# Performance work log

Hardware: AMD Instinct MI355X
Metric: run time of the kernel (lower is better)

## Reference

```python
import jax, jax.numpy as jnp
import numpy as np

B, N, DIM = 16, 784, 512
H, KD, VD = 8, 64, 256  # num_heads, key_dim, val_dim (attn_ratio=4)
RES = 28
EPS = 1e-5
SCALE = KD ** -0.5


def _make_bias_idxs():
    # pos: [2, N] grid coordinates; rel_pos[0]*RES + rel_pos[1]
    yy, xx = np.meshgrid(np.arange(RES), np.arange(RES), indexing='ij')
    pos = np.stack([yy.reshape(-1), xx.reshape(-1)])  # [2, N]
    rel = np.abs(pos[:, :, None] - pos[:, None, :])   # [2, N, N]
    return jnp.asarray(rel[0] * RES + rel[1], dtype=jnp.int32)


def _bn(x, gamma, beta, mean, var):
    return (x - mean) * (gamma * jax.lax.rsqrt(var + EPS)) + beta


def setup_inputs() -> dict:
    key = jax.random.key(0)
    ks = jax.random.split(key, 12)
    qkv_out = (2 * KD + VD) * H  # 3072
    return {
        'x': jax.random.normal(ks[0], (B, N, DIM), jnp.float32),
        'qkv_w': jax.random.normal(ks[1], (qkv_out, DIM), jnp.float32) * (DIM ** -0.5),
        'qkv_gamma': jax.random.uniform(ks[2], (qkv_out,), jnp.float32, 0.5, 1.5),
        'qkv_beta': jax.random.normal(ks[3], (qkv_out,), jnp.float32) * 0.1,
        'qkv_mean': jax.random.normal(ks[4], (qkv_out,), jnp.float32) * 0.1,
        'qkv_var': jax.random.uniform(ks[5], (qkv_out,), jnp.float32, 0.5, 1.5),
        'attention_biases': jax.random.normal(ks[6], (H, RES * RES), jnp.float32) * 0.02,
        'proj_w': jax.random.normal(ks[7], (DIM, VD * H), jnp.float32) * ((VD * H) ** -0.5),
        'proj_gamma': jax.random.uniform(ks[8], (DIM,), jnp.float32, 0.5, 1.5),
        'proj_beta': jax.random.normal(ks[9], (DIM,), jnp.float32) * 0.1,
        'proj_mean': jax.random.normal(ks[10], (DIM,), jnp.float32) * 0.1,
        'proj_var': jax.random.uniform(ks[11], (DIM,), jnp.float32, 0.5, 1.5),
        'bias_idxs': _make_bias_idxs(),
    }


def reference(x, qkv_w, qkv_gamma, qkv_beta, qkv_mean, qkv_var,
              attention_biases, proj_w, proj_gamma, proj_beta,
              proj_mean, proj_var, bias_idxs):
    # QKV: Linear (no bias) + BatchNorm1d (eval/fused form)
    qkv = _bn(jnp.einsum('bnc,oc->bno', x, qkv_w),
              qkv_gamma, qkv_beta, qkv_mean, qkv_var)        # [B, N, 3072]
    qkv = qkv.reshape(B, N, H, 2 * KD + VD)
    q = qkv[..., :KD].transpose(0, 2, 1, 3)                  # [B, H, N, KD]
    k = qkv[..., KD:2 * KD].transpose(0, 2, 1, 3)            # [B, H, N, KD]
    v = qkv[..., 2 * KD:].transpose(0, 2, 1, 3)              # [B, H, N, VD]

    bias = attention_biases[:, bias_idxs]                    # [H, N, N]
    attn = jnp.einsum('bhnd,bhmd->bhnm', q, k) * SCALE + bias
    attn = jax.nn.softmax(attn, axis=-1)
    out = jnp.einsum('bhnm,bhmd->bhnd', attn, v)             # [B, H, N, VD]
    out = out.transpose(0, 2, 1, 3).reshape(B, N, H * VD)    # [B, N, 2048]

    # proj: SiLU -> Linear (no bias) -> BN (eval/fused form)
    out = jax.nn.silu(out)
    out = _bn(jnp.einsum('bnv,cv->bnc', out, proj_w),
              proj_gamma, proj_beta, proj_mean, proj_var)    # [B, N, DIM]
    return out
```

## Files before the change

kernel.cpp:

```cpp
#include <hip/hip_runtime.h>

#define Bsz 16
#define Nseq 784
#define DIM 512
#define NH 8
#define KD 64
#define VD 256
#define QKV_OUT 3072
#define HV 2048
#define NN 614656

typedef __attribute__((ext_vector_type(8))) short short8;
typedef __attribute__((ext_vector_type(4))) float floatx4;

#define OSTR 136

#if __has_builtin(__builtin_amdgcn_exp2f)
#define EXP2(x) __builtin_amdgcn_exp2f(x)
#else
#define EXP2(x) exp2f(x)
#endif

__device__ __forceinline__ unsigned short f2bf(float f) {
  union { float f; unsigned u; } v; v.f = f;
  unsigned r = v.u + 0x7fffu + ((v.u >> 16) & 1u);
  return (unsigned short)(r >> 16);
}
__device__ __forceinline__ float bf2f(unsigned short u) {
  union { unsigned u; float f; } v; v.u = ((unsigned)u) << 16;
  return v.f;
}

__device__ __forceinline__ void glds16(const unsigned short* g, unsigned short* l) {
  __builtin_amdgcn_global_load_lds(
      (const __attribute__((address_space(1))) void*)g,
      (__attribute__((address_space(3))) void*)l, 16, 0, 0);
}

#define N4X 1605632
#define N4Q 393216
#define N4P 262144
__global__ void cvt_all_kernel(const float* __restrict__ x,
                               const float* __restrict__ qw,
                               const float* __restrict__ pw,
                               unsigned short* __restrict__ xb,
                               unsigned short* __restrict__ wq,
                               unsigned short* __restrict__ wp) {
  int i = blockIdx.x * 256 + threadIdx.x;
  const float4* s; ushort4* d; int off;
  if (i < N4X)              { s = (const float4*)x;  d = (ushort4*)xb; off = i; }
  else if (i < N4X + N4Q)   { s = (const float4*)qw; d = (ushort4*)wq; off = i - N4X; }
  else if (i < N4X + N4Q + N4P) { s = (const float4*)pw; d = (ushort4*)wp; off = i - N4X - N4Q; }
  else return;
  float4 v = s[off];
  ushort4 o;
  o.x = f2bf(v.x); o.y = f2bf(v.y); o.z = f2bf(v.z); o.w = f2bf(v.w);
  d[off] = o;
}

__global__ void bias_pre_kernel(const float* __restrict__ biases,
                                const int* __restrict__ bias_idxs,
                                unsigned short* __restrict__ bias_tab) {
  int t = blockIdx.x * 256 + threadIdx.x;
  if (t >= NN) return;
  int idx = bias_idxs[t];
  for (int h = 0; h < NH; ++h)
    bias_tab[(size_t)h * NN + t] = f2bf(biases[h * Nseq + idx]);
}

__global__ __launch_bounds__(256, 2) void qkv_gemm_kernel(
    const unsigned short* __restrict__ A,
    const unsigned short* __restrict__ Bw,
    const float* __restrict__ gamma, const float* __restrict__ beta,
    const float* __restrict__ mean,  const float* __restrict__ var,
    unsigned short* __restrict__ qo,
    unsigned short* __restrict__ ko,
    unsigned short* __restrict__ vto)
{
  const int K = DIM;
  __shared__ unsigned short smem[128 * OSTR];
  int tid = threadIdx.x;
  int wave = tid >> 6, lane = tid & 63;
  int quad = lane >> 4, l16 = lane & 15;
  int wm = wave >> 1, wn = wave & 1;
  int m0 = blockIdx.y * 128, n0 = blockIdx.x * 128;

  int srow = wave * 32 + (lane >> 2);
  int sch = (lane & 3) * 8;
  const unsigned short* Ab = A + (size_t)(m0 + srow) * K + sch;
  const unsigned short* Bb = Bw + (size_t)(n0 + srow) * K + sch;
  unsigned short* AsW = &smem[wave * 1024];
  unsigned short* BsW = &smem[4096 + wave * 1024];

  floatx4 acc[4][4];
  for (int i = 0; i < 4; ++i)
    for (int j = 0; j < 4; ++j) acc[i][j] = (floatx4)0.0f;

  glds16(Ab, AsW);
  glds16(Ab + 16 * K, AsW + 512);
  glds16(Bb, BsW);
  glds16(Bb + 16 * K, BsW + 512);

  for (int k = 0; k < 16; ++k) {
    int cur = k & 1, nb = cur ^ 1;
    __builtin_amdgcn_s_waitcnt(0xC07F);
    __builtin_amdgcn_s_barrier();
    int k0n = ((k + 1) & 15) * 32;
    glds16(Ab + k0n, AsW + nb * 8192);
    glds16(Ab + k0n + 16 * K, AsW + nb * 8192 + 512);
    glds16(Bb + k0n, BsW + nb * 8192);
    glds16(Bb + k0n + 16 * K, BsW + nb * 8192 + 512);
    __builtin_amdgcn_s_waitcnt(0x0F74);
    __builtin_amdgcn_s_barrier();

    const unsigned short* As = &smem[cur * 8192];
    const unsigned short* Bs = &smem[4096 + cur * 8192];
    short8 af[4], bfr[4];
    for (int mt = 0; mt < 4; ++mt)
      af[mt] = *(const short8*)&As[(wm * 64 + mt * 16 + l16) * 32 + quad * 8];
    for (int nt = 0; nt < 4; ++nt)
      bfr[nt] = *(const short8*)&Bs[(wn * 64 + nt * 16 + l16) * 32 + quad * 8];
    for (int mt = 0; mt < 4; ++mt)
      for (int nt = 0; nt < 4; ++nt)
        acc[mt][nt] = __builtin_amdgcn_mfma_f32_16x16x32_bf16(af[mt], bfr[nt], acc[mt][nt], 0, 0, 0);
  }

  int tt = n0 % 384;
  int h = n0 / 384;
  __builtin_amdgcn_s_waitcnt(0x0070);
  __syncthreads();

  if (tt == 0) {
    for (int nt = 0; nt < 4; ++nt) {
      int o = n0 + wn * 64 + nt * 16 + l16;
      float sc = gamma[o] * rsqrtf(var[o] + 1e-5f);
      float bb = beta[o] - mean[o] * sc;
      if (wn == 0) { sc *= 0.125f; bb *= 0.125f; }
      int jl = wn * 64 + nt * 16 + l16;
      for (int mt = 0; mt < 4; ++mt)
        for (int r = 0; r < 4; ++r) {
          int ml = wm * 64 + mt * 16 + quad * 4 + r;
          smem[ml * OSTR + jl] = f2bf(acc[mt][nt][r] * sc + bb);
        }
    }
    __syncthreads();
    for (int i = 0; i < 8; ++i) {
      int c = i * 256 + tid;
      int ml = c >> 4, jc = c & 15;
      int m = m0 + ml;
      int b = m / 784, n = m - b * 784;
      uint4 v = *(uint4*)&smem[ml * OSTR + jc * 8];
      int j = jc * 8;
      if (j < 64) *(uint4*)&qo[(((size_t)b * NH + h) * Nseq + n) * KD + j] = v;
      else        *(uint4*)&ko[(((size_t)b * NH + h) * Nseq + n) * KD + (j - 64)] = v;
    }
  } else {
    for (int nt = 0; nt < 4; ++nt) {
      int o = n0 + wn * 64 + nt * 16 + l16;
      float sc = gamma[o] * rsqrtf(var[o] + 1e-5f);
      float bb = beta[o] - mean[o] * sc;
      int cl = wn * 64 + nt * 16 + l16;
      for (int mt = 0; mt < 4; ++mt)
        for (int r = 0; r < 4; ++r) {
          int ml = wm * 64 + mt * 16 + quad * 4 + r;
          smem[cl * OSTR + ml] = f2bf(acc[mt][nt][r] * sc + bb);
        }
    }
    __syncthreads();
    int cbase = tt - 128;
    for (int i = 0; i < 8; ++i) {
      int c = i * 256 + tid;
      int cl = c >> 4, mc = c & 15;
      int m = m0 + mc * 8;
      int b = m / 784, n = m - b * 784;
      uint4 v = *(uint4*)&smem[cl * OSTR + mc * 8];
      *(uint4*)&vto[(((size_t)b * NH + h) * VD + cbase + cl) * Nseq + n] = v;
    }
  }
}

__global__ __launch_bounds__(512, 2) void attn_kernel(
    const unsigned short* __restrict__ qb,
    const unsigned short* __restrict__ kb,
    const unsigned short* __restrict__ vtb,
    const unsigned short* __restrict__ bias_tab,
    unsigned short* __restrict__ U)
{
  __shared__ unsigned short vt_lds[2 * 256 * 64];
  __shared__ unsigned short k_lds[2 * 64 * 64];
  __shared__ unsigned short bs_lds[2 * 128 * 64];
  __shared__ unsigned short ps_lds[8 * 16 * 64];
  int tid = threadIdx.x;
  int wave = tid >> 6, lane = tid & 63;
  int quad = lane >> 4, l16 = lane & 15;

  int L = blockIdx.x;
  int xcd = L & 7;
  int s = L >> 3;
  int qp = s % 7;
  int bg = s / 7;
  int bh = bg * 8 + xcd;
  int b = bg, h = xcd;
  int row_base = qp * 128 + wave * 16;

  const unsigned short* brow = bias_tab + (size_t)h * NN;

  int lc = lane >> 3;
  int lch = (lane & 7) ^ lc;
  int sw = l16 & 7;

  const unsigned short* vsrc[4];
#pragma unroll
  for (int t = 0; t < 4; ++t)
    vsrc[t] = vtb + ((size_t)bh * VD + t * 64 + wave * 8 + lc) * Nseq + lch * 8;
  const unsigned short* ksrc =
      kb + (size_t)bh * (Nseq * KD) + (wave * 8 + lc) * KD + lch * 8;
  const unsigned short* bsrc[2];
#pragma unroll
  for (int t = 0; t < 2; ++t) {
    int ig = qp * 128 + t * 64 + wave * 8 + lc;
    if (ig > Nseq - 1) ig = Nseq - 1;
    bsrc[t] = brow + (size_t)ig * Nseq + lch * 8;
  }

  short8 qf[2];
  {
    int qrow = row_base + l16;
    const unsigned short* qp_ = qb + ((size_t)bh * Nseq + qrow) * KD;
    qf[0] = *(const short8*)(qp_ + quad * 8);
    qf[1] = *(const short8*)(qp_ + 32 + quad * 8);
  }

#pragma unroll
  for (int t = 0; t < 4; ++t)
    glds16(vsrc[t], &vt_lds[(t * 64 + wave * 8) * 64]);
  glds16(ksrc, &k_lds[wave * 512]);
#pragma unroll
  for (int t = 0; t < 2; ++t)
    glds16(bsrc[t], &bs_lds[(t * 64 + wave * 8) * 64]);

  float lsum = 0.0f;
  floatx4 oacc[16];
#pragma unroll
  for (int ct = 0; ct < 16; ++ct) oacc[ct] = (floatx4)0.0f;

  unsigned short* psW = &ps_lds[wave * 1024];

  for (int kt = 0; kt < 13; ++kt) {
    int cur = kt & 1;
    int nb = cur ^ 1;
    __builtin_amdgcn_s_waitcnt(0xC07F);
    __builtin_amdgcn_s_barrier();

    int ktn = kt + 1; if (ktn >= 13) ktn = 0;
#pragma unroll
    for (int t = 0; t < 4; ++t)
      glds16(vsrc[t] + ktn * 64, &vt_lds[nb * 16384 + (t * 64 + wave * 8) * 64]);
    glds16(ksrc + (size_t)ktn * 4096, &k_lds[nb * 4096 + wave * 512]);
#pragma unroll
    for (int t = 0; t < 2; ++t)
      glds16(bsrc[t] + ktn * 64, &bs_lds[nb * 8192 + (t * 64 + wave * 8) * 64]);

    __builtin_amdgcn_s_waitcnt(0x0F77);
    __builtin_amdgcn_s_barrier();

    const unsigned short* kbuf = &k_lds[cur * 4096];
    const unsigned short* vbuf = &vt_lds[cur * 16384];
    const unsigned short* bbuf = &bs_lds[cur * 8192];

    floatx4 st[4];
#pragma unroll
    for (int jt = 0; jt < 4; ++jt) {
      int row = jt * 16 + l16;
      short8 kf0 = *(const short8*)&kbuf[row * 64 + (quad ^ sw) * 8];
      short8 kf1 = *(const short8*)&kbuf[row * 64 + ((quad + 4) ^ sw) * 8];
      st[jt] = (floatx4)0.0f;
      st[jt] = __builtin_amdgcn_mfma_f32_16x16x32_bf16(kf0, qf[0], st[jt], 0, 0, 0);
      st[jt] = __builtin_amdgcn_mfma_f32_16x16x32_bf16(kf1, qf[1], st[jt], 0, 0, 0);
    }

    bool tail = (kt == 12);
#pragma unroll
    for (int jt = 0; jt < 4; ++jt) {
      int ch = ((jt << 1) + (quad >> 1)) ^ sw;
      int half = (quad & 1) * 4;
      ushort4 bv = *(const ushort4*)&bbuf[(wave * 16 + l16) * 64 + ch * 8 + half];
      float p0 = EXP2((st[jt][0] + bf2f(bv.x)) * 1.44269504f);
      float p1 = EXP2((st[jt][1] + bf2f(bv.y)) * 1.44269504f);
      float p2 = EXP2((st[jt][2] + bf2f(bv.z)) * 1.44269504f);
      float p3 = EXP2((st[jt][3] + bf2f(bv.w)) * 1.44269504f);
      if (tail && jt > 0) { p0 = 0.0f; p1 = 0.0f; p2 = 0.0f; p3 = 0.0f; }
      lsum += (p0 + p1) + (p2 + p3);
      unsigned lo = (unsigned)f2bf(p0) | ((unsigned)f2bf(p1) << 16);
      unsigned hi = (unsigned)f2bf(p2) | ((unsigned)f2bf(p3) << 16);
      *(uint2*)&psW[l16 * 64 + ch * 8 + half] = make_uint2(lo, hi);
    }

#pragma unroll
    for (int ks = 0; ks < 2; ++ks) {
      short8 pf = *(const short8*)&psW[l16 * 64 + ((ks * 4 + quad) ^ sw) * 8];
#pragma unroll
      for (int ct = 0; ct < 16; ++ct) {
        int c = ct * 16 + l16;
        short8 vf = *(const short8*)&vbuf[c * 64 + ((ks * 4 + quad) ^ sw) * 8];
        oacc[ct] = __builtin_amdgcn_mfma_f32_16x16x32_bf16(pf, vf, oacc[ct], 0, 0, 0);
      }
    }
  }

  __builtin_amdgcn_s_waitcnt(0x0070);

  float tot = lsum;
  tot += __shfl_xor(tot, 16);
  tot += __shfl_xor(tot, 32);
  float inv[4];
#pragma unroll
  for (int r = 0; r < 4; ++r) {
    float lr = __shfl(tot, (lane & 48) | (quad * 4 + r));
    inv[r] = 1.0f / lr;
  }
#pragma unroll
  for (int r = 0; r < 4; ++r) {
    int ig = row_base + quad * 4 + r;
    if (ig >= Nseq) continue;
    size_t base = ((size_t)b * Nseq + ig) * HV + h * VD;
#pragma unroll
    for (int ct = 0; ct < 16; ++ct) {
      float u = oacc[ct][r] * inv[r];
      float sg = 1.0f / (1.0f + EXP2(-u * 1.44269504f));
      U[base + ct * 16 + l16] = f2bf(u * sg);
    }
  }
}

__global__ __launch_bounds__(256, 2) void proj_gemm_kernel(
    const unsigned short* __restrict__ Ubuf,
    const unsigned short* __restrict__ Wp,
    const float* __restrict__ gamma, const float* __restrict__ beta,
    const float* __restrict__ mean,  const float* __restrict__ var,
    float* __restrict__ out)
{
  const int K = HV;
  __shared__ unsigned short smem[16384];
  int tid = threadIdx.x;
  int wave = tid >> 6, lane = tid & 63;
  int quad = lane >> 4, l16 = lane & 15;
  int wm = wave >> 1, wn = wave & 1;
  int o0 = blockIdx.y * 128, mB = blockIdx.x * 128;

  int srow = wave * 32 + (lane >> 2);
  int sch = (lane & 3) * 8;
  const unsigned short* Ab = Wp + (size_t)(o0 + srow) * K + sch;
  const unsigned short* Bb = Ubuf + (size_t)(mB + srow) * K + sch;
  unsigned short* AsW = &smem[wave * 1024];
  unsigned short* BsW = &smem[4096 + wave * 1024];

  floatx4 acc[4][4];
  for (int i = 0; i < 4; ++i)
    for (int j = 0; j < 4; ++j) acc[i][j] = (floatx4)0.0f;

  glds16(Ab, AsW);
  glds16(Ab + 16 * K, AsW + 512);
  glds16(Bb, BsW);
  glds16(Bb + 16 * K, BsW + 512);

  for (int k = 0; k < 64; ++k) {
    int cur = k & 1, nb = cur ^ 1;
    __builtin_amdgcn_s_waitcnt(0xC07F);
    __builtin_amdgcn_s_barrier();
    int k0n = ((k + 1) & 63) * 32;
    glds16(Ab + k0n, AsW + nb * 8192);
    glds16(Ab + k0n + 16 * K, AsW + nb * 8192 + 512);
    glds16(Bb + k0n, BsW + nb * 8192);
    glds16(Bb + k0n + 16 * K, BsW + nb * 8192 + 512);
    __builtin_amdgcn_s_waitcnt(0x0F74);
    __builtin_amdgcn_s_barrier();

    const unsigned short* As = &smem[cur * 8192];
    const unsigned short* Bs = &smem[4096 + cur * 8192];
    short8 af[4], bfr[4];
    for (int mt = 0; mt < 4; ++mt)
      af[mt] = *(const short8*)&As[(wm * 64 + mt * 16 + l16) * 32 + quad * 8];
    for (int nt = 0; nt < 4; ++nt)
      bfr[nt] = *(const short8*)&Bs[(wn * 64 + nt * 16 + l16) * 32 + quad * 8];
    for (int mt = 0; mt < 4; ++mt)
      for (int nt = 0; nt < 4; ++nt)
        acc[mt][nt] = __builtin_amdgcn_mfma_f32_16x16x32_bf16(af[mt], bfr[nt], acc[mt][nt], 0, 0, 0);
  }
  __builtin_amdgcn_s_waitcnt(0x0070);

  for (int mt = 0; mt < 4; ++mt) {
    int ob = o0 + wm * 64 + mt * 16 + quad * 4;
    float4 g = *(const float4*)&gamma[ob];
    float4 vr = *(const float4*)&var[ob];
    float4 mn = *(const float4*)&mean[ob];
    float4 bt = *(const float4*)&beta[ob];
    float sc0 = g.x * rsqrtf(vr.x + 1e-5f), bb0 = bt.x - mn.x * sc0;
    float sc1 = g.y * rsqrtf(vr.y + 1e-5f), bb1 = bt.y - mn.y * sc1;
    float sc2 = g.z * rsqrtf(vr.z + 1e-5f), bb2 = bt.z - mn.z * sc2;
    float sc3 = g.w * rsqrtf(vr.w + 1e-5f), bb3 = bt.w - mn.w * sc3;
    for (int nt = 0; nt < 4; ++nt) {
      int m = mB + wn * 64 + nt * 16 + l16;
      float4 v;
      v.x = acc[mt][nt][0] * sc0 + bb0;
      v.y = acc[mt][nt][1] * sc1 + bb1;
      v.z = acc[mt][nt][2] * sc2 + bb2;
      v.w = acc[mt][nt][3] * sc3 + bb3;
      *(float4*)&out[(size_t)m * DIM + ob] = v;
    }
  }
}

extern "C" void kernel_launch(void* const* d_in, const int* in_sizes, int n_in,
                              void* d_out, int out_size, void* d_ws, size_t ws_size,
                              hipStream_t stream) {
  const float* x          = (const float*)d_in[0];
  const float* qkv_w      = (const float*)d_in[1];
  const float* qkv_gamma  = (const float*)d_in[2];
  const float* qkv_beta   = (const float*)d_in[3];
  const float* qkv_mean   = (const float*)d_in[4];
  const float* qkv_var    = (const float*)d_in[5];
  const float* att_biases = (const float*)d_in[6];
  const float* proj_w     = (const float*)d_in[7];
  const float* proj_gamma = (const float*)d_in[8];
  const float* proj_beta  = (const float*)d_in[9];
  const float* proj_mean  = (const float*)d_in[10];
  const float* proj_var   = (const float*)d_in[11];
  const int*   bias_idxs  = (const int*)d_in[12];
  float* out = (float*)d_out;

  char* ws = (char*)d_ws;
  unsigned short* xb  = (unsigned short*)(ws);
  unsigned short* bias_tab = (unsigned short*)(ws);
  unsigned short* wq  = (unsigned short*)(ws + 12845056);
  unsigned short* wp  = (unsigned short*)(ws + 15990784);
  unsigned short* qo  = (unsigned short*)(ws + 18087936);
  unsigned short* ko  = (unsigned short*)(ws + 30932992);
  unsigned short* vto = (unsigned short*)(ws + 43778048);
  unsigned short* Ub  = (unsigned short*)(ws + 95158272);

  {
    int n4 = N4X + N4Q + N4P;
    cvt_all_kernel<<<(n4 + 255) / 256, 256, 0, stream>>>(x, qkv_w, proj_w, xb, wq, wp);
  }

  qkv_gemm_kernel<<<dim3(QKV_OUT / 128, (Bsz * Nseq) / 128), 256, 0, stream>>>(
      xb, wq, qkv_gamma, qkv_beta, qkv_mean, qkv_var, qo, ko, vto);

  bias_pre_kernel<<<(NN + 255) / 256, 256, 0, stream>>>(att_biases, bias_idxs, bias_tab);

  attn_kernel<<<7 * Bsz * NH, 512, 0, stream>>>(qo, ko, vto, bias_tab, Ub);

  proj_gemm_kernel<<<dim3((Bsz * Nseq) / 128, DIM / 128), 256, 0, stream>>>(
      Ub, wp, proj_gamma, proj_beta, proj_mean, proj_var, out);
}
```

Before: 337.2 us.

## Restructure attention kernel around 32x32x16 MFMA with register-resident probabilities

Rewrites the attention kernel to use 4 waves of 32 query rows each with 32x32x16 bf16 MFMAs. The probabilities now stay in registers as the B operand instead of round-tripping through LDS. Bias values are loaded straight from global memory into registers and double-buffered across iterations, and they seed the score accumulator. The log2(e) factor is folded into the precomputed bias and the Q scale, so the exponent needs only an exp2. Packing uses v_cvt_pk_bf16_f32. In exchange the block shrinks from 512 to 256 threads and register pressure per wave rises.

```diff
diff --git a/kernel.cpp b/kernel.cpp
--- a/kernel.cpp
+++ b/kernel.cpp
@@ -11,7 +11,10 @@
 #define NN 614656
 
 typedef __attribute__((ext_vector_type(8))) short short8;
+typedef __attribute__((ext_vector_type(4))) short short4v;
 typedef __attribute__((ext_vector_type(4))) float floatx4;
+typedef __attribute__((ext_vector_type(16))) float f32x16;
+typedef __attribute__((ext_vector_type(2))) unsigned u32x2;
 
 #define OSTR 136
 
@@ -26,9 +29,11 @@
   unsigned r = v.u + 0x7fffu + ((v.u >> 16) & 1u);
   return (unsigned short)(r >> 16);
 }
-__device__ __forceinline__ float bf2f(unsigned short u) {
-  union { unsigned u; float f; } v; v.u = ((unsigned)u) << 16;
-  return v.f;
+__device__ __forceinline__ float bfLO(unsigned u) {
+  union { unsigned u; float f; } v; v.u = u << 16; return v.f;
+}
+__device__ __forceinline__ float bfHI(unsigned u) {
+  union { unsigned u; float f; } v; v.u = u & 0xffff0000u; return v.f;
 }
 
 __device__ __forceinline__ void glds16(const unsigned short* g, unsigned short* l) {
@@ -65,7 +70,7 @@
   if (t >= NN) return;
   int idx = bias_idxs[t];
   for (int h = 0; h < NH; ++h)
-    bias_tab[(size_t)h * NN + t] = f2bf(biases[h * Nseq + idx]);
+    bias_tab[(size_t)h * NN + t] = f2bf(1.44269504f * biases[h * Nseq + idx]);
 }
 
 __global__ __launch_bounds__(256, 2) void qkv_gemm_kernel(
@@ -135,7 +140,7 @@
       int o = n0 + wn * 64 + nt * 16 + l16;
       float sc = gamma[o] * rsqrtf(var[o] + 1e-5f);
       float bb = beta[o] - mean[o] * sc;
-      if (wn == 0) { sc *= 0.125f; bb *= 0.125f; }
+      if (wn == 0) { sc *= 0.18033688f; bb *= 0.18033688f; }
       int jl = wn * 64 + nt * 16 + l16;
       for (int mt = 0; mt < 4; ++mt)
         for (int r = 0; r < 4; ++r) {
@@ -179,7 +184,7 @@
   }
 }
 
-__global__ __launch_bounds__(512, 2) void attn_kernel(
+__global__ __launch_bounds__(256, 2) void attn_kernel(
     const unsigned short* __restrict__ qb,
     const unsigned short* __restrict__ kb,
     const unsigned short* __restrict__ vtb,
@@ -188,11 +193,9 @@
 {
   __shared__ unsigned short vt_lds[2 * 256 * 64];
   __shared__ unsigned short k_lds[2 * 64 * 64];
-  __shared__ unsigned short bs_lds[2 * 128 * 64];
-  __shared__ unsigned short ps_lds[8 * 16 * 64];
   int tid = threadIdx.x;
   int wave = tid >> 6, lane = tid & 63;
-  int quad = lane >> 4, l16 = lane & 15;
+  int lo = lane & 31, hi = lane >> 5;
 
   int L = blockIdx.x;
   int xcd = L & 7;
@@ -201,135 +204,151 @@
   int bg = s / 7;
   int bh = bg * 8 + xcd;
   int b = bg, h = xcd;
-  int row_base = qp * 128 + wave * 16;
-
-  const unsigned short* brow = bias_tab + (size_t)h * NN;
+
+  int qrow_g = qp * 128 + wave * 32 + lo;
+  int qrow = qrow_g < Nseq ? qrow_g : Nseq - 1;
 
   int lc = lane >> 3;
   int lch = (lane & 7) ^ lc;
-  int sw = l16 & 7;
-
-  const unsigned short* vsrc[4];
-#pragma unroll
-  for (int t = 0; t < 4; ++t)
-    vsrc[t] = vtb + ((size_t)bh * VD + t * 64 + wave * 8 + lc) * Nseq + lch * 8;
-  const unsigned short* ksrc =
-      kb + (size_t)bh * (Nseq * KD) + (wave * 8 + lc) * KD + lch * 8;
-  const unsigned short* bsrc[2];
-#pragma unroll
-  for (int t = 0; t < 2; ++t) {
-    int ig = qp * 128 + t * 64 + wave * 8 + lc;
-    if (ig > Nseq - 1) ig = Nseq - 1;
-    bsrc[t] = brow + (size_t)ig * Nseq + lch * 8;
-  }
-
-  short8 qf[2];
+  int swz = lo & 7;
+
+  const unsigned short* vsrc = vtb + ((size_t)bh * VD + wave * 64 + lc) * Nseq + lch * 8;
+  const unsigned short* ksrc = kb + ((size_t)bh * Nseq + wave * 16 + lc) * KD + lch * 8;
+  const unsigned short* brow = bias_tab + (size_t)h * NN + (size_t)qrow * Nseq + hi * 4;
+
+  short8 qf[4];
   {
-    int qrow = row_base + l16;
-    const unsigned short* qp_ = qb + ((size_t)bh * Nseq + qrow) * KD;
-    qf[0] = *(const short8*)(qp_ + quad * 8);
-    qf[1] = *(const short8*)(qp_ + 32 + quad * 8);
-  }
-
-#pragma unroll
-  for (int t = 0; t < 4; ++t)
-    glds16(vsrc[t], &vt_lds[(t * 64 + wave * 8) * 64]);
-  glds16(ksrc, &k_lds[wave * 512]);
-#pragma unroll
-  for (int t = 0; t < 2; ++t)
-    glds16(bsrc[t], &bs_lds[(t * 64 + wave * 8) * 64]);
-
+    const unsigned short* qp_ = qb + ((size_t)bh * Nseq + qrow) * KD + hi * 8;
+#pragma unroll
+    for (int kst = 0; kst < 4; ++kst) qf[kst] = *(const short8*)(qp_ + kst * 16);
+  }
+
+#pragma unroll
+  for (int i = 0; i < 8; ++i) glds16(vsrc + i * (8 * Nseq), &vt_lds[wave * 4096 + i * 512]);
+  glds16(ksrc, &k_lds[wave * 1024]);
+  glds16(ksrc + 8 * KD, &k_lds[wave * 1024 + 512]);
+  u32x2 bvC[8], bvN[8];
+#pragma unroll
+  for (int t = 0; t < 8; ++t) bvC[t] = *(const u32x2*)(brow + t * 8);
+
+  f32x16 oacc[8];
+#pragma unroll
+  for (int ct = 0; ct < 8; ++ct) oacc[ct] = (f32x16)0.0f;
   float lsum = 0.0f;
-  floatx4 oacc[16];
-#pragma unroll
-  for (int ct = 0; ct < 16; ++ct) oacc[ct] = (floatx4)0.0f;
-
-  unsigned short* psW = &ps_lds[wave * 1024];
 
   for (int kt = 0; kt < 13; ++kt) {
-    int cur = kt & 1;
-    int nb = cur ^ 1;
+    int cur = kt & 1, nb = cur ^ 1;
     __builtin_amdgcn_s_waitcnt(0xC07F);
     __builtin_amdgcn_s_barrier();
-
     int ktn = kt + 1; if (ktn >= 13) ktn = 0;
 #pragma unroll
-    for (int t = 0; t < 4; ++t)
-      glds16(vsrc[t] + ktn * 64, &vt_lds[nb * 16384 + (t * 64 + wave * 8) * 64]);
-    glds16(ksrc + (size_t)ktn * 4096, &k_lds[nb * 4096 + wave * 512]);
-#pragma unroll
-    for (int t = 0; t < 2; ++t)
-      glds16(bsrc[t] + ktn * 64, &bs_lds[nb * 8192 + (t * 64 + wave * 8) * 64]);
-
-    __builtin_amdgcn_s_waitcnt(0x0F77);
-    __builtin_amdgcn_s_barrier();
+    for (int i = 0; i < 8; ++i)
+      glds16(vsrc + i * (8 * Nseq) + ktn * 64, &vt_lds[nb * 16384 + wave * 4096 + i * 512]);
+    glds16(ksrc + ktn * (64 * KD), &k_lds[nb * 4096 + wave * 1024]);
+    glds16(ksrc + ktn * (64 * KD) + 8 * KD, &k_lds[nb * 4096 + wave * 1024 + 512]);
+#pragma unroll
+    for (int t = 0; t < 8; ++t) bvN[t] = *(const u32x2*)(brow + ktn * 64 + t * 8);
+    __builtin_amdgcn_s_waitcnt(0x4F72);
+    __builtin_amdgcn_s_barrier();
+    __builtin_amdgcn_sched_barrier(0);
 
     const unsigned short* kbuf = &k_lds[cur * 4096];
     const unsigned short* vbuf = &vt_lds[cur * 16384];
-    const unsigned short* bbuf = &bs_lds[cur * 8192];
-
-    floatx4 st[4];
-#pragma unroll
-    for (int jt = 0; jt < 4; ++jt) {
-      int row = jt * 16 + l16;
-      short8 kf0 = *(const short8*)&kbuf[row * 64 + (quad ^ sw) * 8];
-      short8 kf1 = *(const short8*)&kbuf[row * 64 + ((quad + 4) ^ sw) * 8];
-      st[jt] = (floatx4)0.0f;
-      st[jt] = __builtin_amdgcn_mfma_f32_16x16x32_bf16(kf0, qf[0], st[jt], 0, 0, 0);
-      st[jt] = __builtin_amdgcn_mfma_f32_16x16x32_bf16(kf1, qf[1], st[jt], 0, 0, 0);
-    }
-
-    bool tail = (kt == 12);
-#pragma unroll
-    for (int jt = 0; jt < 4; ++jt) {
-      int ch = ((jt << 1) + (quad >> 1)) ^ sw;
-      int half = (quad & 1) * 4;
-      ushort4 bv = *(const ushort4*)&bbuf[(wave * 16 + l16) * 64 + ch * 8 + half];
-      float p0 = EXP2((st[jt][0] + bf2f(bv.x)) * 1.44269504f);
-      float p1 = EXP2((st[jt][1] + bf2f(bv.y)) * 1.44269504f);
-      float p2 = EXP2((st[jt][2] + bf2f(bv.z)) * 1.44269504f);
-      float p3 = EXP2((st[jt][3] + bf2f(bv.w)) * 1.44269504f);
-      if (tail && jt > 0) { p0 = 0.0f; p1 = 0.0f; p2 = 0.0f; p3 = 0.0f; }
-      lsum += (p0 + p1) + (p2 + p3);
-      unsigned lo = (unsigned)f2bf(p0) | ((unsigned)f2bf(p1) << 16);
-      unsigned hi = (unsigned)f2bf(p2) | ((unsigned)f2bf(p3) << 16);
-      *(uint2*)&psW[l16 * 64 + ch * 8 + half] = make_uint2(lo, hi);
-    }
-
-#pragma unroll
-    for (int ks = 0; ks < 2; ++ks) {
-      short8 pf = *(const short8*)&psW[l16 * 64 + ((ks * 4 + quad) ^ sw) * 8];
-#pragma unroll
-      for (int ct = 0; ct < 16; ++ct) {
-        int c = ct * 16 + l16;
-        short8 vf = *(const short8*)&vbuf[c * 64 + ((ks * 4 + quad) ^ sw) * 8];
-        oacc[ct] = __builtin_amdgcn_mfma_f32_16x16x32_bf16(pf, vf, oacc[ct], 0, 0, 0);
+
+    f32x16 st0, st1;
+#pragma unroll
+    for (int r = 0; r < 16; ++r) {
+      unsigned c0 = bvC[r >> 2][(r & 3) >> 1];
+      unsigned c1 = bvC[4 + (r >> 2)][(r & 3) >> 1];
+      st0[r] = (r & 1) ? bfHI(c0) : bfLO(c0);
+      st1[r] = (r & 1) ? bfHI(c1) : bfLO(c1);
+    }
+#pragma unroll
+    for (int kst = 0; kst < 4; ++kst) {
+      int ch = ((kst * 2 + hi) ^ swz) * 8;
+      short8 kf0 = *(const short8*)&kbuf[lo * 64 + ch];
+      short8 kf1 = *(const short8*)&kbuf[(32 + lo) * 64 + ch];
+      st0 = __builtin_amdgcn_mfma_f32_32x32x16_bf16(kf0, qf[kst], st0, 0, 0, 0);
+      st1 = __builtin_amdgcn_mfma_f32_32x32x16_bf16(kf1, qf[kst], st1, 0, 0, 0);
+    }
+
+#pragma unroll
+    for (int r = 0; r < 16; ++r) st0[r] = EXP2(st0[r]);
+#pragma unroll
+    for (int r = 0; r < 16; ++r) st1[r] = EXP2(st1[r]);
+    if (kt == 12) {
+#pragma unroll
+      for (int r = 8; r < 16; ++r) st0[r] = 0.0f;
+#pragma unroll
+      for (int r = 0; r < 16; ++r) st1[r] = 0.0f;
+    }
+    {
+      float s0 = (st0[0] + st0[1]) + (st0[2] + st0[3]);
+      float s1 = (st0[4] + st0[5]) + (st0[6] + st0[7]);
+      float s2 = (st0[8] + st0[9]) + (st0[10] + st0[11]);
+      float s3 = (st0[12] + st0[13]) + (st0[14] + st0[15]);
+      float s4 = (st1[0] + st1[1]) + (st1[2] + st1[3]);
+      float s5 = (st1[4] + st1[5]) + (st1[6] + st1[7]);
+      float s6 = (st1[8] + st1[9]) + (st1[10] + st1[11]);
+      float s7 = (st1[12] + st1[13]) + (st1[14] + st1[15]);
+      lsum += ((s0 + s1) + (s2 + s3)) + ((s4 + s5) + (s6 + s7));
+    }
+
+    short8 pf[4];
+#pragma unroll
+    for (int kst = 0; kst < 4; ++kst) {
+      float a0, a1, a2, a3, b0, b1, b2, b3;
+      if (kst == 0)      { a0=st0[0]; a1=st0[1]; a2=st0[2];  a3=st0[3];  b0=st0[4];  b1=st0[5];  b2=st0[6];  b3=st0[7];  }
+      else if (kst == 1) { a0=st0[8]; a1=st0[9]; a2=st0[10]; a3=st0[11]; b0=st0[12]; b1=st0[13]; b2=st0[14]; b3=st0[15]; }
+      else if (kst == 2) { a0=st1[0]; a1=st1[1]; a2=st1[2];  a3=st1[3];  b0=st1[4];  b1=st1[5];  b2=st1[6];  b3=st1[7];  }
+      else               { a0=st1[8]; a1=st1[9]; a2=st1[10]; a3=st1[11]; b0=st1[12]; b1=st1[13]; b2=st1[14]; b3=st1[15]; }
+      unsigned X0, X1, Y0, Y1;
+      asm("v_cvt_pk_bf16_f32 %0, %1, %2" : "=v"(X0) : "v"(a0), "v"(a1));
+      asm("v_cvt_pk_bf16_f32 %0, %1, %2" : "=v"(X1) : "v"(a2), "v"(a3));
+      asm("v_cvt_pk_bf16_f32 %0, %1, %2" : "=v"(Y0) : "v"(b0), "v"(b1));
+      asm("v_cvt_pk_bf16_f32 %0, %1, %2" : "=v"(Y1) : "v"(b2), "v"(b3));
+      union { unsigned u[4]; short8 s; } pk_;
+      pk_.u[0] = X0; pk_.u[1] = X1; pk_.u[2] = Y0; pk_.u[3] = Y1;
+      pf[kst] = pk_.s;
+    }
+
+#pragma unroll
+    for (int kst = 0; kst < 4; ++kst) {
+      int chL = ((kst * 2) ^ swz) * 8 + 4 * hi;
+      int chH = ((kst * 2 + 1) ^ swz) * 8 + 4 * hi;
+#pragma unroll
+      for (int ct = 0; ct < 8; ++ct) {
+        const unsigned short* vr = &vbuf[(ct * 32 + lo) * 64];
+        union { short4v half[2]; short8 s; } vv;
+        vv.half[0] = *(const short4v*)&vr[chL];
+        vv.half[1] = *(const short4v*)&vr[chH];
+        oacc[ct] = __builtin_amdgcn_mfma_f32_32x32x16_bf16(vv.s, pf[kst], oacc[ct], 0, 0, 0);
       }
     }
+
+#pragma unroll
+    for (int t = 0; t < 8; ++t) bvC[t] = bvN[t];
   }
 
   __builtin_amdgcn_s_waitcnt(0x0070);
 
-  float tot = lsum;
-  tot += __shfl_xor(tot, 16);
-  tot += __shfl_xor(tot, 32);
-  float inv[4];
-#pragma unroll
-  for (int r = 0; r < 4; ++r) {
-    float lr = __shfl(tot, (lane & 48) | (quad * 4 + r));
-    inv[r] = 1.0f / lr;
-  }
-#pragma unroll
-  for (int r = 0; r < 4; ++r) {
-    int ig = row_base + quad * 4 + r;
-    if (ig >= Nseq) continue;
-    size_t base = ((size_t)b * Nseq + ig) * HV + h * VD;
-#pragma unroll
-    for (int ct = 0; ct < 16; ++ct) {
-      float u = oacc[ct][r] * inv[r];
-      float sg = 1.0f / (1.0f + EXP2(-u * 1.44269504f));
-      U[base + ct * 16 + l16] = f2bf(u * sg);
-    }
+  float tot = lsum + __shfl_xor(lsum, 32);
+  float inv = 1.0f / tot;
+  if (qrow_g < Nseq) {
+    size_t base = ((size_t)b * Nseq + qrow_g) * HV + h * VD;
+#pragma unroll
+    for (int ct = 0; ct < 8; ++ct)
+#pragma unroll
+      for (int g2 = 0; g2 < 4; ++g2) {
+        ushort4 o4;
+#pragma unroll
+        for (int r4 = 0; r4 < 4; ++r4) {
+          float u = oacc[ct][g2 * 4 + r4] * inv;
+          float sg = 1.0f / (1.0f + EXP2(-u * 1.44269504f));
+          ((unsigned short*)&o4)[r4] = f2bf(u * sg);
+        }
+        *(ushort4*)&U[base + ct * 32 + g2 * 8 + hi * 4] = o4;
+      }
   }
 }
 
@@ -449,7 +468,7 @@
 
   bias_pre_kernel<<<(NN + 255) / 256, 256, 0, stream>>>(att_biases, bias_idxs, bias_tab);
 
-  attn_kernel<<<7 * Bsz * NH, 512, 0, stream>>>(qo, ko, vto, bias_tab, Ub);
+  attn_kernel<<<7 * Bsz * NH, 256, 0, stream>>>(qo, ko, vto, bias_tab, Ub);
 
   proj_gemm_kernel<<<dim3((Bsz * Nseq) / 128, DIM / 128), 256, 0, stream>>>(
       Ub, wp, proj_gamma, proj_beta, proj_mean, proj_var, out);
```

New measurement: 309.3 us. 1.09x faster.
